# Kernel tuning notes

Measured on AMD Instinct MI355X. Metric: run time of the kernel, lower is better.

Reference implementation:

```python
import jax, jax.numpy as jnp
import numpy as np

INF = 1e9
EPS = 1e-5

def layer_norm(x, g, b):
    mu = jnp.mean(x, axis=-1, keepdims=True)
    var = jnp.mean(jnp.square(x - mu), axis=-1, keepdims=True)
    return (x - mu) * jax.lax.rsqrt(var + EPS) * g + b

def setup_inputs() -> dict:
    key = jax.random.key(0)
    ks = jax.random.split(key, 12)
    B, S, N = 1, 512, 384
    c_in, c_hid, c_z, H = 64, 32, 128, 8
    d = c_hid * H
    sc = lambda fan: 1.0 / np.sqrt(fan)
    return {
        "m": jax.random.normal(ks[0], (B, S, N, c_in), jnp.float32),
        "z": jax.random.normal(ks[1], (B, N, N, c_z), jnp.float32),
        "mask": jnp.ones((B, N, N), jnp.float32),
        "gamma_m": jnp.ones((c_in,), jnp.float32),
        "beta_m": jnp.zeros((c_in,), jnp.float32),
        "gamma_z": jnp.ones((c_z,), jnp.float32),
        "beta_z": jnp.zeros((c_z,), jnp.float32),
        "w_z": jax.random.normal(ks[2], (c_z, H), jnp.float32) * sc(c_z),
        "b_z": jnp.zeros((H,), jnp.float32),
        "w_v": jax.random.normal(ks[3], (c_in, d), jnp.float32) * sc(c_in),
        "b_v": jnp.zeros((d,), jnp.float32),
        "w_g": jax.random.normal(ks[4], (c_in, d), jnp.float32) * sc(c_in),
        "b_g": jnp.zeros((d,), jnp.float32),
        "w_o": jax.random.normal(ks[5], (d, c_in), jnp.float32) * sc(d),
        "b_o": jnp.zeros((c_in,), jnp.float32),
    }

def reference(m, z, mask, gamma_m, beta_m, gamma_z, beta_z,
              w_z, b_z, w_v, b_v, w_g, b_g, w_o, b_o):
    B, S, N, c_in = m.shape
    H = w_z.shape[-1]
    C = w_v.shape[-1] // H
    # pair branch: LN -> linear -> [B,H,Nq,Nk] logits + mask bias -> softmax
    zn = layer_norm(z, gamma_z, beta_z)
    logits = jnp.einsum('bqkz,zh->bhqk', zn, w_z) + b_z[None, :, None, None]
    logits = logits + (INF * (mask - 1.0))[:, None, :, :]
    w = jax.nn.softmax(logits, axis=-1)                      # [B,H,Nq,Nk]
    # MSA branch: LN -> value / gate projections
    mn = layer_norm(m, gamma_m, beta_m)
    v = (mn @ w_v + b_v).reshape(B, S, N, H, C)              # [B,S,Nk,H,C]
    o = jnp.einsum('bhqk,bskhc->bsqhc', w, v)                # broadcast over S
    g = jax.nn.sigmoid(mn @ w_g + b_g).reshape(B, S, N, H, C)
    out = (o * g).reshape(B, S, N, H * C) @ w_o + b_o
    return out
```

## Files before the change

kernel.cpp:

```cpp
#include <hip/hip_runtime.h>
#include <hip/hip_bf16.h>

#define INFV 1e9f
#define EPSV 1e-5f

typedef unsigned short u16;
typedef unsigned int u32;
typedef __attribute__((ext_vector_type(8))) short short8;
typedef __attribute__((ext_vector_type(4))) float float4v;

__device__ __forceinline__ u16 f2us(float f) {
    u32 v;
    __builtin_memcpy(&v, &f, 4);
    u32 r = v + 0x7fffu + ((v >> 16) & 1u);
    return (u16)(r >> 16);
}

__device__ __forceinline__ float wred_sum(float x) {
    #pragma unroll
    for (int o = 32; o; o >>= 1) x += __shfl_xor(x, o);
    return x;
}
__device__ __forceinline__ float wred_max(float x) {
    #pragma unroll
    for (int o = 32; o; o >>= 1) x = fmaxf(x, __shfl_xor(x, o));
    return x;
}

__global__ __launch_bounds__(256) void k_prep_ln(
    const float* __restrict__ m, const float* __restrict__ gm, const float* __restrict__ bm,
    u16* __restrict__ mn,
    const float* __restrict__ wv, const float* __restrict__ wg,
    const float* __restrict__ wo, const float* __restrict__ wz,
    u16* __restrict__ wv_t, u16* __restrict__ wg_t,
    u16* __restrict__ wo_t, u16* __restrict__ wzT)
{
    if (blockIdx.x < 12288) {
        const int tid  = threadIdx.x;
        const int wid  = tid >> 6;
        const int lane = tid & 63;
        const int rloc = lane >> 4;
        const int c4   = (lane & 15) * 4;
        const int row  = blockIdx.x * 16 + wid * 4 + rloc;
        const float4 x = *(const float4*)(m + (size_t)row * 64 + c4);
        float s1 = x.x + x.y + x.z + x.w;
        float s2 = x.x * x.x + x.y * x.y + x.z * x.z + x.w * x.w;
        #pragma unroll
        for (int o = 8; o; o >>= 1) { s1 += __shfl_xor(s1, o); s2 += __shfl_xor(s2, o); }
        const float mean = s1 * (1.0f / 64.0f);
        const float var  = s2 * (1.0f / 64.0f) - mean * mean;
        const float rs   = rsqrtf(var + EPSV);
        const float4 g = *(const float4*)(gm + c4);
        const float4 b = *(const float4*)(bm + c4);
        uint2 pk;
        pk.x = (u32)f2us((x.x - mean) * rs * g.x + b.x) | ((u32)f2us((x.y - mean) * rs * g.y + b.y) << 16);
        pk.y = (u32)f2us((x.z - mean) * rs * g.z + b.z) | ((u32)f2us((x.w - mean) * rs * g.w + b.w) << 16);
        *(uint2*)(mn + (size_t)row * 64 + c4) = pk;
    } else {
        const int i = (blockIdx.x - 12288) * 256 + threadIdx.x;
        if (i < 16384) {
            const int n = i >> 6, k = i & 63;
            wv_t[i] = f2us(wv[(size_t)k * 256 + n]);
        } else if (i < 32768) {
            const int j = i - 16384, n = j >> 6, k = j & 63;
            wg_t[j] = f2us(wg[(size_t)k * 256 + n]);
        } else if (i < 49152) {
            const int j = i - 32768, n = j >> 8, k = j & 255;
            wo_t[j] = f2us(wo[(size_t)k * 64 + n]);
        } else if (i < 51200) {
            const int j = i - 49152, n = j >> 7, k = j & 127;
            wzT[j] = (n < 8) ? f2us(wz[(size_t)k * 8 + n]) : (u16)0;
        }
    }
}

__global__ __launch_bounds__(256) void k_logits2(
    const float* __restrict__ z, const float* __restrict__ mask,
    const float* __restrict__ gz, const float* __restrict__ bz,
    const u16* __restrict__ wzT, const float* __restrict__ bzb,
    float* __restrict__ wbuf)
{
    const int tid   = threadIdx.x;
    const int wid   = tid >> 6;
    const int lane  = tid & 63;
    const int lrow  = lane & 15;
    const int lkg   = lane >> 4;
    const int pair0 = (blockIdx.x * 4 + wid) * 16;

    float x[4][8];
    float s1 = 0.0f, s2 = 0.0f;
    #pragma unroll
    for (int ks = 0; ks < 4; ks++) {
        const float4* zp = (const float4*)(z + (size_t)(pair0 + lrow) * 128 + ks * 32 + lkg * 8);
        const float4 a = zp[0], b = zp[1];
        x[ks][0] = a.x; x[ks][1] = a.y; x[ks][2] = a.z; x[ks][3] = a.w;
        x[ks][4] = b.x; x[ks][5] = b.y; x[ks][6] = b.z; x[ks][7] = b.w;
        #pragma unroll
        for (int j = 0; j < 8; j++) { s1 += x[ks][j]; s2 += x[ks][j] * x[ks][j]; }
    }
    s1 += __shfl_xor(s1, 16); s1 += __shfl_xor(s1, 32);
    s2 += __shfl_xor(s2, 16); s2 += __shfl_xor(s2, 32);
    const float mean = s1 * (1.0f / 128.0f);
    const float var  = s2 * (1.0f / 128.0f) - mean * mean;
    const float rs   = rsqrtf(var + EPSV);

    float4v acc = (float4v){0.f, 0.f, 0.f, 0.f};
    #pragma unroll
    for (int ks = 0; ks < 4; ks++) {
        const int c0 = ks * 32 + lkg * 8;
        const float4 g0 = *(const float4*)(gz + c0);
        const float4 g1 = *(const float4*)(gz + c0 + 4);
        const float4 b0 = *(const float4*)(bz + c0);
        const float4 b1 = *(const float4*)(bz + c0 + 4);
        const float gv[8] = {g0.x, g0.y, g0.z, g0.w, g1.x, g1.y, g1.z, g1.w};
        const float bvv[8] = {b0.x, b0.y, b0.z, b0.w, b1.x, b1.y, b1.z, b1.w};
        short8 afr;
        #pragma unroll
        for (int j = 0; j < 8; j++)
            afr[j] = (short)f2us((x[ks][j] - mean) * rs * gv[j] + bvv[j]);
        const short8 bfr = *(const short8*)(wzT + (size_t)lrow * 128 + c0);
        acc = __builtin_amdgcn_mfma_f32_16x16x32_bf16(afr, bfr, acc, 0, 0, 0);
    }
    if (lrow < 8) {
        const float bzv = bzb[lrow];
        #pragma unroll
        for (int r = 0; r < 4; r++) {
            const int p = pair0 + lkg * 4 + r;
            const float mb = INFV * (mask[p] - 1.0f);
            wbuf[(size_t)lrow * 147456 + p] = acc[r] + bzv + mb;
        }
    }
}

__global__ __launch_bounds__(256) void k_softmax(
    const float* __restrict__ wbuf, u16* __restrict__ wb16)
{
    const int r = blockIdx.x * 4 + (threadIdx.x >> 6);
    const int lane = threadIdx.x & 63;
    const float* base = wbuf + (size_t)r * 384;
    float v[6];
    float mx = -1e30f;
    #pragma unroll
    for (int j = 0; j < 6; j++) {
        v[j] = base[lane + j * 64];
        mx = fmaxf(mx, v[j]);
    }
    mx = wred_max(mx);
    float s = 0.0f;
    #pragma unroll
    for (int j = 0; j < 6; j++) {
        v[j] = __expf(v[j] - mx);
        s += v[j];
    }
    s = wred_sum(s);
    const float inv = 1.0f / s;
    u16* ob = wb16 + (size_t)r * 384;
    #pragma unroll
    for (int j = 0; j < 6; j++) ob[lane + j * 64] = f2us(v[j] * inv);
}

__global__ __launch_bounds__(256, 2) void k_fused4(
    const u16* __restrict__ mn,
    const float* __restrict__ bv, const float* __restrict__ bg, const float* __restrict__ bo,
    const u16* __restrict__ wv_t, const u16* __restrict__ wg_t, const u16* __restrict__ wo_t,
    const u16* __restrict__ wb16, float* __restrict__ out)
{
    __shared__ __align__(16) char smem[67584];
    u16* vtt = (u16*)smem;
    u16* og  = (u16*)smem;

    const int tid  = threadIdx.x;
    const int wid  = tid >> 6;
    const int lane = tid & 63;
    const int lrow = lane & 15;
    const int lkg  = lane >> 4;
    const int s    = blockIdx.y;
    const int q0   = blockIdx.x * 128;

    const int vmt  = wid & 1;
    const int vnt0 = (wid >> 1) * 8;

    float4v oacc[32];
    #pragma unroll
    for (int mt = 0; mt < 2; mt++)
        #pragma unroll
        for (int nt = 0; nt < 16; nt++) {
            const float b = bv[nt * 16 + lrow];
            oacc[mt * 16 + nt] = (float4v){b, b, b, b};
        }

    for (int kt = 0; kt < 12; kt++) {
        const int k0 = kt * 32;
        float4v vacc[8];
        #pragma unroll
        for (int nt = 0; nt < 8; nt++) vacc[nt] = (float4v){0.f, 0.f, 0.f, 0.f};
        const u16* mnk = mn + ((size_t)s * 384 + k0 + vmt * 16 + lrow) * 64;
        #pragma unroll
        for (int ks = 0; ks < 2; ks++) {
            const short8 a = *(const short8*)(mnk + ks * 32 + lkg * 8);
            #pragma unroll
            for (int nt = 0; nt < 8; nt++) {
                const short8 b = *(const short8*)(wv_t + (size_t)((vnt0 + nt) * 16 + lrow) * 64 + ks * 32 + lkg * 8);
                vacc[nt] = __builtin_amdgcn_mfma_f32_16x16x32_bf16(a, b, vacc[nt], 0, 0, 0);
            }
        }
        u16* vb = vtt + (size_t)(kt & 1) * 8192;
        const int kg8 = vmt * 2 + (lkg >> 1);
        const int ko  = (lkg & 1) * 4;
        #pragma unroll
        for (int nt = 0; nt < 8; nt++) {
            uint2 pk;
            pk.x = (u32)f2us(vacc[nt][0]) | ((u32)f2us(vacc[nt][1]) << 16);
            pk.y = (u32)f2us(vacc[nt][2]) | ((u32)f2us(vacc[nt][3]) << 16);
            *(uint2*)&vb[((size_t)kg8 * 256 + (vnt0 + nt) * 16 + lrow) * 8 + ko] = pk;
        }
        __syncthreads();

        short8 ah[2][8];
        #pragma unroll
        for (int mt = 0; mt < 2; mt++)
            #pragma unroll
            for (int h = 0; h < 8; h++)
                ah[mt][h] = *(const short8*)(wb16 + (size_t)h * 147456
                              + (size_t)(q0 + wid * 32 + mt * 16 + lrow) * 384 + k0 + lkg * 8);
        #pragma unroll
        for (int nt = 0; nt < 16; nt++) {
            const short8 b = *(const short8*)&vb[((size_t)lkg * 256 + nt * 16 + lrow) * 8];
            oacc[nt]      = __builtin_amdgcn_mfma_f32_16x16x32_bf16(ah[0][nt >> 1], b, oacc[nt], 0, 0, 0);
            oacc[16 + nt] = __builtin_amdgcn_mfma_f32_16x16x32_bf16(ah[1][nt >> 1], b, oacc[16 + nt], 0, 0, 0);
        }
    }
    __syncthreads();

    #pragma unroll
    for (int mt = 0; mt < 2; mt++) {
        const u16* mnq = mn + ((size_t)s * 384 + q0 + wid * 32 + mt * 16 + lrow) * 64;
        const short8 a0 = *(const short8*)(mnq + lkg * 8);
        const short8 a1 = *(const short8*)(mnq + 32 + lkg * 8);
        #pragma unroll
        for (int nt = 0; nt < 16; nt++) {
            const float bgv = bg[nt * 16 + lrow];
            float4v gacc = (float4v){bgv, bgv, bgv, bgv};
            const short8 b0 = *(const short8*)(wg_t + (size_t)(nt * 16 + lrow) * 64 + lkg * 8);
            const short8 b1 = *(const short8*)(wg_t + (size_t)(nt * 16 + lrow) * 64 + 32 + lkg * 8);
            gacc = __builtin_amdgcn_mfma_f32_16x16x32_bf16(a0, b0, gacc, 0, 0, 0);
            gacc = __builtin_amdgcn_mfma_f32_16x16x32_bf16(a1, b1, gacc, 0, 0, 0);
            #pragma unroll
            for (int r = 0; r < 4; r++) {
                const float sg = 1.0f / (1.0f + __expf(-gacc[r]));
                og[(size_t)(wid * 32 + mt * 16 + lkg * 4 + r) * 264 + nt * 16 + lrow]
                    = f2us(oacc[mt * 16 + nt][r] * sg);
            }
        }
    }
    __syncthreads();

    #pragma unroll
    for (int mt = 0; mt < 2; mt++) {
        short8 af[8];
        #pragma unroll
        for (int ks = 0; ks < 8; ks++)
            af[ks] = *(const short8*)&og[(size_t)(wid * 32 + mt * 16 + lrow) * 264 + ks * 32 + lkg * 8];
        #pragma unroll
        for (int nt = 0; nt < 4; nt++) {
            const float bov = bo[nt * 16 + lrow];
            float4v fac = (float4v){bov, bov, bov, bov};
            #pragma unroll
            for (int ks = 0; ks < 8; ks++) {
                const short8 b = *(const short8*)(wo_t + (size_t)(nt * 16 + lrow) * 256 + ks * 32 + lkg * 8);
                fac = __builtin_amdgcn_mfma_f32_16x16x32_bf16(af[ks], b, fac, 0, 0, 0);
            }
            #pragma unroll
            for (int r = 0; r < 4; r++)
                out[((size_t)s * 384 + q0 + wid * 32 + mt * 16 + lkg * 4 + r) * 64 + nt * 16 + lrow]
                    = fac[r];
        }
    }
}

extern "C" void kernel_launch(void* const* d_in, const int* in_sizes, int n_in,
                              void* d_out, int out_size, void* d_ws, size_t ws_size,
                              hipStream_t stream) {
    const float* m    = (const float*)d_in[0];
    const float* z    = (const float*)d_in[1];
    const float* mask = (const float*)d_in[2];
    const float* gm   = (const float*)d_in[3];
    const float* bm   = (const float*)d_in[4];
    const float* gz   = (const float*)d_in[5];
    const float* bz   = (const float*)d_in[6];
    const float* wz   = (const float*)d_in[7];
    const float* bzb  = (const float*)d_in[8];
    const float* wv   = (const float*)d_in[9];
    const float* bv   = (const float*)d_in[10];
    const float* wg   = (const float*)d_in[11];
    const float* bg   = (const float*)d_in[12];
    const float* wo   = (const float*)d_in[13];
    const float* bo   = (const float*)d_in[14];
    float* out = (float*)d_out;

    char* ws = (char*)d_ws;
    float* wbuf = (float*)ws;
    u16*  wb16  = (u16*)(ws + 4718592);
    u16*  mn    = (u16*)(ws + 7077888);
    u16*  wv_t  = (u16*)(ws + 32243712);
    u16*  wg_t  = (u16*)(ws + 32276480);
    u16*  wo_t  = (u16*)(ws + 32309248);
    u16*  wzT   = (u16*)(ws + 32342016);

    k_prep_ln<<<12488, 256, 0, stream>>>(m, gm, bm, mn, wv, wg, wo, wz, wv_t, wg_t, wo_t, wzT);
    k_logits2<<<2304,  256, 0, stream>>>(z, mask, gz, bz, wzT, bzb, wbuf);
    k_softmax<<<768,   256, 0, stream>>>(wbuf, wb16);
    k_fused4 <<<dim3(3, 512), 256, 0, stream>>>(mn, bv, bg, bo, wv_t, wg_t, wo_t, wb16, out);
}
```

Before: 461.9 us.

## Precompute V projection once per sequence in separate kernel instead of per q-block

The value projection (mn @ w_v) was previously recomputed inside each of the three q-block workgroups per sequence row and staged through shared memory with a barrier each k-step. It is now computed once by a new kernel into a transposed bf16 global buffer (about 100 MB), which the fused kernel reads directly from global memory. This removes a threefold redundant GEMM and the per-iteration __syncthreads. The cost is a large extra write and read of V through HBM/L2 and one more kernel launch.

```diff
diff --git a/kernel.cpp b/kernel.cpp
--- a/kernel.cpp
+++ b/kernel.cpp
@@ -112,7 +112,7 @@
         const float4 g1 = *(const float4*)(gz + c0 + 4);
         const float4 b0 = *(const float4*)(bz + c0);
         const float4 b1 = *(const float4*)(bz + c0 + 4);
-        const float gv[8] = {g0.x, g0.y, g0.z, g0.w, g1.x, g1.y, g1.z, g1.w};
+        const float gv[8]  = {g0.x, g0.y, g0.z, g0.w, g1.x, g1.y, g1.z, g1.w};
         const float bvv[8] = {b0.x, b0.y, b0.z, b0.w, b1.x, b1.y, b1.z, b1.w};
         short8 afr;
         #pragma unroll
@@ -159,15 +159,51 @@
     for (int j = 0; j < 6; j++) ob[lane + j * 64] = f2us(v[j] * inv);
 }
 
-__global__ __launch_bounds__(256, 2) void k_fused4(
+__global__ __launch_bounds__(256) void k_vt(
+    const u16* __restrict__ mn, const u16* __restrict__ wv_t,
+    u16* __restrict__ v_t)
+{
+    const int tid  = threadIdx.x;
+    const int wid  = tid >> 6;
+    const int lane = tid & 63;
+    const int lrow = lane & 15;
+    const int lkg  = lane >> 4;
+    const int s    = blockIdx.x / 12;
+    const int k0   = (blockIdx.x % 12) * 32;
+
+    const int vmt  = wid & 1;
+    const int vnt0 = (wid >> 1) * 8;
+
+    float4v vacc[8];
+    #pragma unroll
+    for (int nt = 0; nt < 8; nt++) vacc[nt] = (float4v){0.f, 0.f, 0.f, 0.f};
+    const u16* mnk = mn + ((size_t)s * 384 + k0 + vmt * 16 + lrow) * 64;
+    #pragma unroll
+    for (int ks = 0; ks < 2; ks++) {
+        const short8 a = *(const short8*)(mnk + ks * 32 + lkg * 8);
+        #pragma unroll
+        for (int nt = 0; nt < 8; nt++) {
+            const short8 b = *(const short8*)(wv_t + (size_t)((vnt0 + nt) * 16 + lrow) * 64 + ks * 32 + lkg * 8);
+            vacc[nt] = __builtin_amdgcn_mfma_f32_16x16x32_bf16(a, b, vacc[nt], 0, 0, 0);
+        }
+    }
+    #pragma unroll
+    for (int nt = 0; nt < 8; nt++) {
+        uint2 pk;
+        pk.x = (u32)f2us(vacc[nt][0]) | ((u32)f2us(vacc[nt][1]) << 16);
+        pk.y = (u32)f2us(vacc[nt][2]) | ((u32)f2us(vacc[nt][3]) << 16);
+        *(uint2*)(v_t + ((size_t)s * 256 + (vnt0 + nt) * 16 + lrow) * 384 + k0 + vmt * 16 + lkg * 4) = pk;
+    }
+}
+
+__global__ __launch_bounds__(256, 2) void k_fused6(
     const u16* __restrict__ mn,
     const float* __restrict__ bv, const float* __restrict__ bg, const float* __restrict__ bo,
-    const u16* __restrict__ wv_t, const u16* __restrict__ wg_t, const u16* __restrict__ wo_t,
-    const u16* __restrict__ wb16, float* __restrict__ out)
-{
-    __shared__ __align__(16) char smem[67584];
-    u16* vtt = (u16*)smem;
-    u16* og  = (u16*)smem;
+    const u16* __restrict__ wg_t, const u16* __restrict__ wo_t,
+    const u16* __restrict__ v_t, const u16* __restrict__ wb16,
+    float* __restrict__ out)
+{
+    __shared__ __align__(16) u16 og[128 * 264];
 
     const int tid  = threadIdx.x;
     const int wid  = tid >> 6;
@@ -177,8 +213,7 @@
     const int s    = blockIdx.y;
     const int q0   = blockIdx.x * 128;
 
-    const int vmt  = wid & 1;
-    const int vnt0 = (wid >> 1) * 8;
+    const u16* vts = v_t + (size_t)s * 98304;
 
     float4v oacc[32];
     #pragma unroll
@@ -191,31 +226,6 @@
 
     for (int kt = 0; kt < 12; kt++) {
         const int k0 = kt * 32;
-        float4v vacc[8];
-        #pragma unroll
-        for (int nt = 0; nt < 8; nt++) vacc[nt] = (float4v){0.f, 0.f, 0.f, 0.f};
-        const u16* mnk = mn + ((size_t)s * 384 + k0 + vmt * 16 + lrow) * 64;
-        #pragma unroll
-        for (int ks = 0; ks < 2; ks++) {
-            const short8 a = *(const short8*)(mnk + ks * 32 + lkg * 8);
-            #pragma unroll
-            for (int nt = 0; nt < 8; nt++) {
-                const short8 b = *(const short8*)(wv_t + (size_t)((vnt0 + nt) * 16 + lrow) * 64 + ks * 32 + lkg * 8);
-                vacc[nt] = __builtin_amdgcn_mfma_f32_16x16x32_bf16(a, b, vacc[nt], 0, 0, 0);
-            }
-        }
-        u16* vb = vtt + (size_t)(kt & 1) * 8192;
-        const int kg8 = vmt * 2 + (lkg >> 1);
-        const int ko  = (lkg & 1) * 4;
-        #pragma unroll
-        for (int nt = 0; nt < 8; nt++) {
-            uint2 pk;
-            pk.x = (u32)f2us(vacc[nt][0]) | ((u32)f2us(vacc[nt][1]) << 16);
-            pk.y = (u32)f2us(vacc[nt][2]) | ((u32)f2us(vacc[nt][3]) << 16);
-            *(uint2*)&vb[((size_t)kg8 * 256 + (vnt0 + nt) * 16 + lrow) * 8 + ko] = pk;
-        }
-        __syncthreads();
-
         short8 ah[2][8];
         #pragma unroll
         for (int mt = 0; mt < 2; mt++)
@@ -225,12 +235,11 @@
                               + (size_t)(q0 + wid * 32 + mt * 16 + lrow) * 384 + k0 + lkg * 8);
         #pragma unroll
         for (int nt = 0; nt < 16; nt++) {
-            const short8 b = *(const short8*)&vb[((size_t)lkg * 256 + nt * 16 + lrow) * 8];
+            const short8 b = *(const short8*)(vts + (size_t)(nt * 16 + lrow) * 384 + k0 + lkg * 8);
             oacc[nt]      = __builtin_amdgcn_mfma_f32_16x16x32_bf16(ah[0][nt >> 1], b, oacc[nt], 0, 0, 0);
             oacc[16 + nt] = __builtin_amdgcn_mfma_f32_16x16x32_bf16(ah[1][nt >> 1], b, oacc[16 + nt], 0, 0, 0);
         }
     }
-    __syncthreads();
 
     #pragma unroll
     for (int mt = 0; mt < 2; mt++) {
@@ -297,18 +306,20 @@
     const float* wo   = (const float*)d_in[13];
     const float* bo   = (const float*)d_in[14];
     float* out = (float*)d_out;
-
     char* ws = (char*)d_ws;
-    float* wbuf = (float*)ws;
-    u16*  wb16  = (u16*)(ws + 4718592);
-    u16*  mn    = (u16*)(ws + 7077888);
-    u16*  wv_t  = (u16*)(ws + 32243712);
-    u16*  wg_t  = (u16*)(ws + 32276480);
-    u16*  wo_t  = (u16*)(ws + 32309248);
-    u16*  wzT   = (u16*)(ws + 32342016);
+
+    u16*  wb16 = (u16*)ws;
+    u16*  mn   = (u16*)(ws + 2359296);
+    u16*  v_t  = (u16*)(ws + 27525120);
+    float* wbuf = (float*)(ws + 27525120);
+    u16*  wv_t = (u16*)(ws + 128188416);
+    u16*  wg_t = (u16*)(ws + 128221184);
+    u16*  wo_t = (u16*)(ws + 128253952);
+    u16*  wzT  = (u16*)(ws + 128286720);
 
     k_prep_ln<<<12488, 256, 0, stream>>>(m, gm, bm, mn, wv, wg, wo, wz, wv_t, wg_t, wo_t, wzT);
     k_logits2<<<2304,  256, 0, stream>>>(z, mask, gz, bz, wzT, bzb, wbuf);
     k_softmax<<<768,   256, 0, stream>>>(wbuf, wb16);
-    k_fused4 <<<dim3(3, 512), 256, 0, stream>>>(mn, bv, bg, bo, wv_t, wg_t, wo_t, wb16, out);
-}
+    k_vt     <<<6144,  256, 0, stream>>>(mn, wv_t, v_t);
+    k_fused6 <<<dim3(3, 512), 256, 0, stream>>>(mn, bv, bg, bo, wg_t, wo_t, v_t, wb16, out);
+}
```

After: 605.9 us. +31.2%, slower.
